# Kernel tuning notes

Hardware: AMD Instinct MI355X
Metric: run time of the kernel (lower is better)

The kernel has to match this reference:

```python
import jax, jax.numpy as jnp
import numpy as np

D_MODEL, D_K, D_V, H = 1024, 64, 64, 16
B, N = 4, 2048


def setup_inputs() -> dict:
    key = jax.random.key(0)
    ks = jax.random.split(key, 11)
    s = 0.02
    return {
        "Q": jax.random.normal(ks[0], (B, N, D_MODEL), jnp.float32),
        "K": jax.random.normal(ks[1], (B, N, D_MODEL), jnp.float32),
        "V": jax.random.normal(ks[2], (B, N, D_MODEL), jnp.float32),
        # stacked per-head projection weights: [h, d_model, d_k]
        "Wq": jax.random.normal(ks[3], (H, D_MODEL, D_K), jnp.float32) * s,
        "bq": jax.random.normal(ks[4], (H, D_K), jnp.float32) * s,
        "Wk": jax.random.normal(ks[5], (H, D_MODEL, D_K), jnp.float32) * s,
        "bk": jax.random.normal(ks[6], (H, D_K), jnp.float32) * s,
        "Wv": jax.random.normal(ks[7], (H, D_MODEL, D_V), jnp.float32) * s,
        "bv": jax.random.normal(ks[8], (H, D_V), jnp.float32) * s,
        "Wo": jax.random.normal(ks[9], (H * D_V, D_MODEL), jnp.float32) * s,
        "bo": jax.random.normal(ks[10], (D_MODEL,), jnp.float32) * s,
        "apply_mask": 1,
    }


def reference(Q, K, V, Wq, bq, Wk, bk, Wv, bv, Wo, bo, apply_mask):
    # fused per-head projections: [b, h, n, d_k]
    q = jnp.einsum("bnd,hdk->bhnk", Q, Wq) + bq[None, :, None, :]
    k = jnp.einsum("bnd,hdk->bhnk", K, Wk) + bk[None, :, None, :]
    v = jnp.einsum("bnd,hdv->bhnv", V, Wv) + bv[None, :, None, :]
    scores = jnp.einsum("bhnk,bhmk->bhnm", q, k) / jnp.sqrt(
        jnp.asarray(D_K, q.dtype)
    )
    if apply_mask:
        n = Q.shape[1]
        causal = jnp.tril(jnp.ones((n, n), dtype=bool))
        scores = jnp.where(causal[None, None], scores, -jnp.inf)
    weights = jax.nn.softmax(scores, axis=-1)
    out = jnp.einsum("bhnm,bhmv->bhnv", weights, v)
    # concat heads: [b, n, h*d_v]
    out = out.transpose(0, 2, 1, 3).reshape(Q.shape[0], Q.shape[1], H * D_V)
    return out @ Wo + bo
```

## Files before the change

### kernel.cpp

```cpp
#include <hip/hip_runtime.h>
#include <hip/hip_bf16.h>

#define H 16
#define DM 1024
#define DK 64
#define B_ 4
#define N_ 2048

typedef __attribute__((ext_vector_type(8))) short bf16x8;
typedef __attribute__((ext_vector_type(4))) short s16x4;
typedef __attribute__((ext_vector_type(2))) unsigned int u32x2;
typedef __attribute__((ext_vector_type(4))) float f32x4;

static __device__ __forceinline__ short f2bs(float x) {
    __hip_bfloat16 b = __float2bfloat16(x);
    return *reinterpret_cast<short*>(&b);
}

static __device__ __forceinline__ void async16(const void* g, void* l) {
    __builtin_amdgcn_global_load_lds(
        (const __attribute__((address_space(1))) void*)g,
        (__attribute__((address_space(3))) void*)l, 16, 0, 0);
}

static __device__ __forceinline__ unsigned packbf(float lo, float hi) {
    return __builtin_amdgcn_perm(__float_as_uint(hi), __float_as_uint(lo), 0x07060302u);
}

__global__ __launch_bounds__(256) void prep_kernel(
    const float* __restrict__ Q, const float* __restrict__ K, const float* __restrict__ V,
    const float* __restrict__ Wq, const float* __restrict__ Wk,
    const float* __restrict__ Wv, const float* __restrict__ Wo,
    short* __restrict__ Qb, short* __restrict__ Kb, short* __restrict__ Vb,
    short* __restrict__ wqT, short* __restrict__ wkT,
    short* __restrict__ wvT, short* __restrict__ woT)
{
    int y = blockIdx.y;
    if (y < 3) {
        const float* s = (y == 0) ? Q : (y == 1) ? K : V;
        short* d = (y == 0) ? Qb : (y == 1) ? Kb : Vb;
        size_t i = ((size_t)blockIdx.x * 256 + threadIdx.x) * 8;
        f32x4 a = *(const f32x4*)(s + i);
        f32x4 b = *(const f32x4*)(s + i + 4);
        bf16x8 p;
        #pragma unroll
        for (int j = 0; j < 4; ++j) { p[j] = f2bs(a[j]); p[4 + j] = f2bs(b[j]); }
        *(bf16x8*)(d + i) = p;
        return;
    }
    if (blockIdx.x >= 1024) return;
    __shared__ float tile[64][65];
    int z = blockIdx.x >> 8;
    int bx = blockIdx.x & 255;
    int t = threadIdx.x;
    int tj = t & 63, ti = t >> 6;

    if (z < 3) {
        const float* src = (z == 0) ? Wq : (z == 1) ? Wk : Wv;
        short* dst = (z == 0) ? wqT : (z == 1) ? wkT : wvT;
        int h = bx >> 4;
        int dmt = bx & 15;
        #pragma unroll
        for (int r = 0; r < 16; ++r) {
            int i = r * 4 + ti;
            tile[i][tj] = src[((size_t)h * 1024 + dmt * 64 + i) * 64 + tj];
        }
        __syncthreads();
        #pragma unroll
        for (int r = 0; r < 16; ++r) {
            int dk = r * 4 + ti;
            dst[((size_t)h * 64 + dk) * 1024 + dmt * 64 + tj] = f2bs(tile[tj][dk]);
        }
    } else {
        int kt = bx >> 4;
        int nt = bx & 15;
        #pragma unroll
        for (int r = 0; r < 16; ++r) {
            int i = r * 4 + ti;
            tile[i][tj] = Wo[((size_t)kt * 64 + i) * 1024 + nt * 64 + tj];
        }
        __syncthreads();
        #pragma unroll
        for (int r = 0; r < 16; ++r) {
            int jn = r * 4 + ti;
            woT[((size_t)nt * 64 + jn) * 1024 + kt * 64 + tj] = f2bs(tile[tj][jn]);
        }
    }
}

static __device__ __forceinline__ void gemm_mainloop(
    const short* __restrict__ A, const short* __restrict__ BT,
    int rowM0, int colN0, char* lds, f32x4 (&acc)[4][4])
{
    int tid = threadIdx.x;
    int lane = tid & 63, w = tid >> 6;
    int l16 = lane & 15, quad = lane >> 4;
    int wm = w >> 1, wn = w & 1;
    int xg = (quad ^ ((l16 >> 1) & 3)) << 4;

    int r0 = w * 32 + (lane >> 2);
    int gsl = ((lane & 3) ^ ((lane >> 3) & 3)) << 4;
    int dst0 = w * 2048 + lane * 16;
    const char* Ag0 = (const char*)A + (size_t)(rowM0 + r0) * 2048 + gsl;
    const char* Ag1 = Ag0 + 16 * 2048;
    const char* Bg0 = (const char*)BT + (size_t)(colN0 + r0) * 2048 + gsl;
    const char* Bg1 = Bg0 + 16 * 2048;

    #pragma unroll
    for (int t = 0; t < 2; ++t) {
        size_t kb = (size_t)t * 64;
        char* As = lds + t * 16384;
        char* Bs = As + 8192;
        async16(Ag0 + kb, As + dst0);
        async16(Ag1 + kb, As + dst0 + 1024);
        async16(Bg0 + kb, Bs + dst0);
        async16(Bg1 + kb, Bs + dst0 + 1024);
    }

    int c0 = 0;
    int cr = 32768;
    for (int it = 0; it < 32; ++it) {
        if (it < 31) asm volatile("s_waitcnt vmcnt(4)" ::: "memory");
        else         asm volatile("s_waitcnt vmcnt(0)" ::: "memory");
        __builtin_amdgcn_s_barrier();
        __builtin_amdgcn_sched_barrier(0);

        if (it + 2 < 32) {
            size_t kb = (size_t)(it + 2) * 64;
            char* Aw = lds + cr;
            char* Bw = Aw + 8192;
            async16(Ag0 + kb, Aw + dst0);
            async16(Ag1 + kb, Aw + dst0 + 1024);
            async16(Bg0 + kb, Bw + dst0);
            async16(Bg1 + kb, Bw + dst0 + 1024);
        }
        __builtin_amdgcn_sched_barrier(0);

        const char* As = lds + c0;
        const char* Bs = As + 8192;
        bf16x8 a[4], b[4];
        #pragma unroll
        for (int i = 0; i < 4; ++i)
            a[i] = *(const bf16x8*)(As + (wm * 64 + i * 16 + l16) * 64 + xg);
        #pragma unroll
        for (int j = 0; j < 4; ++j)
            b[j] = *(const bf16x8*)(Bs + (wn * 64 + j * 16 + l16) * 64 + xg);
        #pragma unroll
        for (int i = 0; i < 4; ++i)
            #pragma unroll
            for (int j = 0; j < 4; ++j)
                acc[i][j] = __builtin_amdgcn_mfma_f32_16x16x32_bf16(a[i], b[j], acc[i][j], 0, 0, 0);

        c0 += 16384; if (c0 == 49152) c0 = 0;
        cr += 16384; if (cr == 49152) cr = 0;
    }
}

__global__ __launch_bounds__(256) void proj_gemm(
    const short* __restrict__ Qb, const short* __restrict__ Kb, const short* __restrict__ Vb,
    const short* __restrict__ wqT, const short* __restrict__ wkT, const short* __restrict__ wvT,
    const float* __restrict__ bq, const float* __restrict__ bk, const float* __restrict__ bv,
    short* __restrict__ qbuf, short* __restrict__ kbuf, short* __restrict__ vTbuf)
{
    __shared__ char lds[49152];
    int which = blockIdx.z;
    const short* A  = (which == 0) ? Qb : (which == 1) ? Kb : Vb;
    const short* BT = (which == 0) ? wqT : (which == 1) ? wkT : wvT;
    const float* bias = (which == 0) ? bq : (which == 1) ? bk : bv;

    int rowM0 = blockIdx.x * 128;
    int colN0 = blockIdx.y * 128;

    f32x4 acc[4][4];
    #pragma unroll
    for (int i = 0; i < 4; ++i)
        #pragma unroll
        for (int j = 0; j < 4; ++j) acc[i][j] = (f32x4){0.f, 0.f, 0.f, 0.f};

    gemm_mainloop(A, BT, rowM0, colN0, lds, acc);

    int lane = threadIdx.x & 63, w = threadIdx.x >> 6;
    int l16 = lane & 15, quad = lane >> 4;
    int wm = w >> 1, wn = w & 1;

    if (which == 2) {
        #pragma unroll
        for (int j = 0; j < 4; ++j) {
            int col = colN0 + wn * 64 + j * 16 + l16;
            int hh = col >> 6, dv = col & 63;
            float bs = bias[col];
            #pragma unroll
            for (int i = 0; i < 4; ++i) {
                int rowb = rowM0 + wm * 64 + i * 16 + quad * 4;
                int bb = rowb >> 11, n0 = rowb & 2047;
                s16x4 pk;
                #pragma unroll
                for (int r2 = 0; r2 < 4; ++r2) pk[r2] = f2bs(acc[i][j][r2] + bs);
                *(s16x4*)(vTbuf + (((size_t)bb * H + hh) * DK + dv) * N_ + n0) = pk;
            }
        }
    } else {
        short* dst = (which == 0) ? qbuf : kbuf;
        float scl = (which == 0) ? 0.180336880f : 1.0f;
        #pragma unroll
        for (int j = 0; j < 4; ++j) {
            int col = colN0 + wn * 64 + j * 16 + l16;
            float bs = bias[col];
            #pragma unroll
            for (int i = 0; i < 4; ++i) {
                int rowb = rowM0 + wm * 64 + i * 16 + quad * 4;
                #pragma unroll
                for (int r2 = 0; r2 < 4; ++r2)
                    dst[(size_t)(rowb + r2) * 1024 + col] = f2bs((acc[i][j][r2] + bs) * scl);
            }
        }
    }
}

__global__ __launch_bounds__(256) void out_gemm(
    const short* __restrict__ obuf, const short* __restrict__ woT,
    const float* __restrict__ bo, float* __restrict__ out)
{
    __shared__ char lds[49152];
    int rowM0 = blockIdx.x * 128;
    int colN0 = blockIdx.y * 128;

    f32x4 acc[4][4];
    #pragma unroll
    for (int i = 0; i < 4; ++i)
        #pragma unroll
        for (int j = 0; j < 4; ++j) acc[i][j] = (f32x4){0.f, 0.f, 0.f, 0.f};

    gemm_mainloop(obuf, woT, rowM0, colN0, lds, acc);

    int lane = threadIdx.x & 63, w = threadIdx.x >> 6;
    int l16 = lane & 15, quad = lane >> 4;
    int wm = w >> 1, wn = w & 1;

    #pragma unroll
    for (int j = 0; j < 4; ++j) {
        int col = colN0 + wn * 64 + j * 16 + l16;
        float bs = bo[col];
        #pragma unroll
        for (int i = 0; i < 4; ++i) {
            int rowb = rowM0 + wm * 64 + i * 16 + quad * 4;
            #pragma unroll
            for (int r2 = 0; r2 < 4; ++r2)
                out[(size_t)(rowb + r2) * 1024 + col] = acc[i][j][r2] + bs;
        }
    }
}

__global__ __launch_bounds__(256) void flash_kernel(
    const short* __restrict__ qbuf, const short* __restrict__ kbuf, const short* __restrict__ vT,
    short* __restrict__ obuf, const int* __restrict__ amask)
{
    __shared__ short Ks[2][4096];
    __shared__ short Vs[2][4096];
    __shared__ char  plds[4][2048];

    int bid = blockIdx.x;
    int g = bid & 7, idx = bid >> 3;
    int bh = g * 8 + (idx >> 4);
    int xq = idx & 15;
    int b = bh >> 4, h = bh & 15;

    int tid = threadIdx.x;
    int lane = tid & 63, wave = tid >> 6;
    int l16 = lane & 15, quad = lane >> 4;
    int msk = amask[0];

    int i8 = lane >> 3, i7 = lane & 7;
    int sg = (i7 ^ i8) << 4;
    int pk0 = i8 * 4 + wave;
    int skey = wave * 16 + i8;
    int ldst = wave * 2048 + lane * 16;

    const char* kbase = (const char*)(kbuf + (size_t)b * 2048 * 1024 + h * 64);
    const char* vbase = (const char*)(vT + ((size_t)(b * 16 + h) * 64) * 2048);

    int m7 = l16 & 7;
    int g0 = (quad ^ m7) << 4;
    int g1 = ((4 | quad) ^ m7) << 4;

    char* pw = plds[wave];
    int prd0 = l16 * 128 + g0;
    int prd1 = l16 * 128 + g1;
    int pwa[4];
    #pragma unroll
    for (int r = 0; r < 4; ++r) {
        int row = quad * 4 + r;
        pwa[r] = row * 128 + (((l16 >> 1) ^ (row & 7)) << 4) + ((l16 & 1) << 3);
    }

    for (int pass = 0; pass < 2; ++pass) {
        int qt = pass ? (31 - xq) : xq;
        int qw = qt * 64 + wave * 16;
        int nkb = msk ? (qt + 1) : 32;

        const short* qp = qbuf + ((size_t)(b * 2048 + qw + l16)) * 1024 + h * 64;
        bf16x8 aq0 = *(const bf16x8*)(qp + quad * 8);
        bf16x8 aq1 = *(const bf16x8*)(qp + 32 + quad * 8);

        f32x4 o[4];
        float lsum[4];
        #pragma unroll
        for (int i = 0; i < 4; ++i) { o[i] = (f32x4){0.f, 0.f, 0.f, 0.f}; lsum[i] = 0.f; }

        async16(kbase + (size_t)pk0 * 2048 + sg, (char*)Ks[0] + ldst);
        async16(kbase + (size_t)(pk0 + 32) * 2048 + sg, (char*)Ks[0] + ldst + 1024);
        async16(vbase + (size_t)skey * 4096 + sg, (char*)Vs[0] + ldst);
        async16(vbase + (size_t)(skey + 8) * 4096 + sg, (char*)Vs[0] + ldst + 1024);

        for (int ib = 0; ib < nkb; ++ib) {
            __syncthreads();
            int cur = ib & 1;
            if (ib + 1 < nkb) {
                int nb = (ib + 1) & 1;
                size_t kb2 = (size_t)(ib + 1) * 64;
                async16(kbase + (kb2 + pk0) * 2048 + sg, (char*)Ks[nb] + ldst);
                async16(kbase + (kb2 + pk0 + 32) * 2048 + sg, (char*)Ks[nb] + ldst + 1024);
                async16(vbase + (size_t)skey * 4096 + kb2 * 2 + sg, (char*)Vs[nb] + ldst);
                async16(vbase + (size_t)(skey + 8) * 4096 + kb2 * 2 + sg, (char*)Vs[nb] + ldst + 1024);
            }
            int kb = ib * 64;

            f32x4 s[4];
            __builtin_amdgcn_s_setprio(1);
            #pragma unroll
            for (int nt = 0; nt < 4; ++nt) {
                const char* kr = (const char*)Ks[cur] + (nt * 16 + l16) * 128;
                bf16x8 b0 = *(const bf16x8*)(kr + g0);
                bf16x8 b1 = *(const bf16x8*)(kr + g1);
                f32x4 t = (f32x4){0.f, 0.f, 0.f, 0.f};
                t = __builtin_amdgcn_mfma_f32_16x16x32_bf16(aq0, b0, t, 0, 0, 0);
                t = __builtin_amdgcn_mfma_f32_16x16x32_bf16(aq1, b1, t, 0, 0, 0);
                s[nt] = t;
            }
            __builtin_amdgcn_s_setprio(0);

            if (msk && (kb + 63 > qw)) {
                #pragma unroll
                for (int r = 0; r < 4; ++r) {
                    int row = qw + quad * 4 + r;
                    #pragma unroll
                    for (int nt = 0; nt < 4; ++nt) {
                        int col = kb + l16 * 4 + nt;
                        if (col > row) s[nt][r] = -3e38f;
                    }
                }
            }

            __builtin_amdgcn_wave_barrier();
            #pragma unroll
            for (int r = 0; r < 4; ++r) {
                float p0 = __builtin_amdgcn_exp2f(s[0][r]);
                float p1 = __builtin_amdgcn_exp2f(s[1][r]);
                float p2 = __builtin_amdgcn_exp2f(s[2][r]);
                float p3 = __builtin_amdgcn_exp2f(s[3][r]);
                lsum[r] += (p0 + p1) + (p2 + p3);
                u32x2 pk;
                pk[0] = packbf(p0, p1);
                pk[1] = packbf(p2, p3);
                *(u32x2*)(pw + pwa[r]) = pk;
            }
            __builtin_amdgcn_wave_barrier();
            bf16x8 ap0 = *(const bf16x8*)(pw + prd0);
            bf16x8 ap1 = *(const bf16x8*)(pw + prd1);
            __builtin_amdgcn_wave_barrier();

            __builtin_amdgcn_s_setprio(1);
            #pragma unroll
            for (int vb = 0; vb < 4; ++vb) {
                const char* vr = (const char*)Vs[cur] + (vb * 16 + l16) * 128;
                bf16x8 v0 = *(const bf16x8*)(vr + g0);
                bf16x8 v1 = *(const bf16x8*)(vr + g1);
                o[vb] = __builtin_amdgcn_mfma_f32_16x16x32_bf16(ap0, v0, o[vb], 0, 0, 0);
                o[vb] = __builtin_amdgcn_mfma_f32_16x16x32_bf16(ap1, v1, o[vb], 0, 0, 0);
            }
            __builtin_amdgcn_s_setprio(0);
        }

        #pragma unroll
        for (int r = 0; r < 4; ++r) {
            float t = lsum[r];
            #pragma unroll
            for (int off = 1; off < 16; off <<= 1) t += __shfl_xor(t, off, 64);
            float inv = 1.0f / t;
            int row = qw + quad * 4 + r;
            #pragma unroll
            for (int vb = 0; vb < 4; ++vb)
                obuf[((size_t)(b * 2048 + row)) * 1024 + h * 64 + vb * 16 + l16] =
                    f2bs(o[vb][r] * inv);
        }
        __syncthreads();
    }
}

extern "C" void kernel_launch(void* const* d_in, const int* in_sizes, int n_in,
                              void* d_out, int out_size, void* d_ws, size_t ws_size,
                              hipStream_t stream)
{
    const float* Q  = (const float*)d_in[0];
    const float* K  = (const float*)d_in[1];
    const float* V  = (const float*)d_in[2];
    const float* Wq = (const float*)d_in[3];
    const float* bq = (const float*)d_in[4];
    const float* Wk = (const float*)d_in[5];
    const float* bk = (const float*)d_in[6];
    const float* Wv = (const float*)d_in[7];
    const float* bv = (const float*)d_in[8];
    const float* Wo = (const float*)d_in[9];
    const float* bo = (const float*)d_in[10];
    const int* amask = (const int*)d_in[11];
    float* out = (float*)d_out;

    char* ws = (char*)d_ws;
    const size_t SZ = (size_t)B_ * N_ * DM * sizeof(short);
    const size_t SZW = (size_t)H * DK * DM * sizeof(short);
    short* Qb    = (short*)ws; ws += SZ;
    short* Kb    = (short*)ws; ws += SZ;
    short* Vb    = (short*)ws; ws += SZ;
    short* qbuf  = (short*)ws; ws += SZ;
    short* kbuf  = (short*)ws; ws += SZ;
    short* vTbuf = (short*)ws; ws += SZ;
    short* wqT   = (short*)ws; ws += SZW;
    short* wkT   = (short*)ws; ws += SZW;
    short* wvT   = (short*)ws; ws += SZW;
    short* woT   = (short*)ws; ws += SZW;
    short* obuf  = Qb;

    prep_kernel<<<dim3(4096, 4), dim3(256), 0, stream>>>(Q, K, V, Wq, Wk, Wv, Wo,
                                                         Qb, Kb, Vb, wqT, wkT, wvT, woT);
    proj_gemm<<<dim3(64, 8, 3), dim3(256), 0, stream>>>(Qb, Kb, Vb, wqT, wkT, wvT,
                                                        bq, bk, bv, qbuf, kbuf, vTbuf);
    flash_kernel<<<dim3(1024), dim3(256), 0, stream>>>(qbuf, kbuf, vTbuf, obuf, amask);
    out_gemm<<<dim3(64, 8), dim3(256), 0, stream>>>(obuf, woT, bo, out);
}
```

Baseline: 314.6 us.

## Use 256x256 tiles with 512-thread blocks for projection GEMM

Replaces the 128x128, 256-thread projection GEMM with a 256x256 tile computed by 8 waves, each owning a 128x64 sub-tile with 8x4 MFMA accumulators. The triple-buffered LDS ring grows to 96 KB. This raises arithmetic intensity per loaded byte and halves global traffic per output. The cost is fewer blocks (384 instead of 1536) on a 256-CU device, more registers per thread, and lower occupancy.

After: 329.5 us. 4.7% more time.

```diff
diff --git a/kernel.cpp b/kernel.cpp
--- a/kernel.cpp
+++ b/kernel.cpp
@@ -84,6 +84,134 @@
         for (int r = 0; r < 16; ++r) {
             int jn = r * 4 + ti;
             woT[((size_t)nt * 64 + jn) * 1024 + kt * 64 + tj] = f2bs(tile[tj][jn]);
+        }
+    }
+}
+
+static __device__ __forceinline__ void gemm_mainloop256(
+    const short* __restrict__ A, const short* __restrict__ BT,
+    int rowM0, int colN0, char* lds, f32x4 (&acc)[8][4])
+{
+    int tid = threadIdx.x;
+    int lane = tid & 63, w = tid >> 6;
+    int l16 = lane & 15, quad = lane >> 4;
+    int wm = w >> 2, wn = w & 3;
+    int xg = (quad ^ ((l16 >> 1) & 3)) << 4;
+
+    int r0 = w * 32 + (lane >> 2);
+    int gsl = ((lane & 3) ^ ((lane >> 3) & 3)) << 4;
+    int dst0 = w * 2048 + lane * 16;
+    const char* Ag0 = (const char*)A + (size_t)(rowM0 + r0) * 2048 + gsl;
+    const char* Ag1 = Ag0 + 16 * 2048;
+    const char* Bg0 = (const char*)BT + (size_t)(colN0 + r0) * 2048 + gsl;
+    const char* Bg1 = Bg0 + 16 * 2048;
+
+    #pragma unroll
+    for (int t = 0; t < 2; ++t) {
+        size_t kb = (size_t)t * 64;
+        char* As = lds + t * 32768;
+        char* Bs = As + 16384;
+        async16(Ag0 + kb, As + dst0);
+        async16(Ag1 + kb, As + dst0 + 1024);
+        async16(Bg0 + kb, Bs + dst0);
+        async16(Bg1 + kb, Bs + dst0 + 1024);
+    }
+
+    int c0 = 0;
+    int cr = 65536;
+    for (int it = 0; it < 32; ++it) {
+        if (it < 31) asm volatile("s_waitcnt vmcnt(4)" ::: "memory");
+        else         asm volatile("s_waitcnt vmcnt(0)" ::: "memory");
+        __builtin_amdgcn_s_barrier();
+        __builtin_amdgcn_sched_barrier(0);
+
+        if (it + 2 < 32) {
+            size_t kb = (size_t)(it + 2) * 64;
+            char* Aw = lds + cr;
+            char* Bw = Aw + 16384;
+            async16(Ag0 + kb, Aw + dst0);
+            async16(Ag1 + kb, Aw + dst0 + 1024);
+            async16(Bg0 + kb, Bw + dst0);
+            async16(Bg1 + kb, Bw + dst0 + 1024);
+        }
+        __builtin_amdgcn_sched_barrier(0);
+
+        const char* As = lds + c0;
+        const char* Bs = As + 16384;
+        bf16x8 b[4];
+        #pragma unroll
+        for (int j = 0; j < 4; ++j)
+            b[j] = *(const bf16x8*)(Bs + (wn * 64 + j * 16 + l16) * 64 + xg);
+        #pragma unroll
+        for (int m = 0; m < 8; ++m) {
+            bf16x8 a = *(const bf16x8*)(As + (wm * 128 + m * 16 + l16) * 64 + xg);
+            #pragma unroll
+            for (int j = 0; j < 4; ++j)
+                acc[m][j] = __builtin_amdgcn_mfma_f32_16x16x32_bf16(a, b[j], acc[m][j], 0, 0, 0);
+        }
+
+        c0 += 32768; if (c0 == 98304) c0 = 0;
+        cr += 32768; if (cr == 98304) cr = 0;
+    }
+}
+
+__global__ __launch_bounds__(512) void proj_gemm(
+    const short* __restrict__ Qb, const short* __restrict__ Kb, const short* __restrict__ Vb,
+    const short* __restrict__ wqT, const short* __restrict__ wkT, const short* __restrict__ wvT,
+    const float* __restrict__ bq, const float* __restrict__ bk, const float* __restrict__ bv,
+    short* __restrict__ qbuf, short* __restrict__ kbuf, short* __restrict__ vTbuf)
+{
+    __shared__ char lds[98304];
+    int which = blockIdx.z;
+    const short* A  = (which == 0) ? Qb : (which == 1) ? Kb : Vb;
+    const short* BT = (which == 0) ? wqT : (which == 1) ? wkT : wvT;
+    const float* bias = (which == 0) ? bq : (which == 1) ? bk : bv;
+
+    int rowM0 = blockIdx.x * 256;
+    int colN0 = blockIdx.y * 256;
+
+    f32x4 acc[8][4];
+    #pragma unroll
+    for (int i = 0; i < 8; ++i)
+        #pragma unroll
+        for (int j = 0; j < 4; ++j) acc[i][j] = (f32x4){0.f, 0.f, 0.f, 0.f};
+
+    gemm_mainloop256(A, BT, rowM0, colN0, lds, acc);
+
+    int lane = threadIdx.x & 63, w = threadIdx.x >> 6;
+    int l16 = lane & 15, quad = lane >> 4;
+    int wm = w >> 2, wn = w & 3;
+
+    if (which == 2) {
+        #pragma unroll
+        for (int j = 0; j < 4; ++j) {
+            int col = colN0 + wn * 64 + j * 16 + l16;
+            int hh = col >> 6, dv = col & 63;
+            float bs = bias[col];
+            #pragma unroll
+            for (int m = 0; m < 8; ++m) {
+                int rowb = rowM0 + wm * 128 + m * 16 + quad * 4;
+                int bb = rowb >> 11, n0 = rowb & 2047;
+                s16x4 pk;
+                #pragma unroll
+                for (int r2 = 0; r2 < 4; ++r2) pk[r2] = f2bs(acc[m][j][r2] + bs);
+                *(s16x4*)(vTbuf + (((size_t)bb * H + hh) * DK + dv) * N_ + n0) = pk;
+            }
+        }
+    } else {
+        short* dst = (which == 0) ? qbuf : kbuf;
+        float scl = (which == 0) ? 0.180336880f : 1.0f;
+        #pragma unroll
+        for (int j = 0; j < 4; ++j) {
+            int col = colN0 + wn * 64 + j * 16 + l16;
+            float bs = bias[col];
+            #pragma unroll
+            for (int m = 0; m < 8; ++m) {
+                int rowb = rowM0 + wm * 128 + m * 16 + quad * 4;
+                #pragma unroll
+                for (int r2 = 0; r2 < 4; ++r2)
+                    dst[(size_t)(rowb + r2) * 1024 + col] = f2bs((acc[m][j][r2] + bs) * scl);
+            }
         }
     }
 }
@@ -153,67 +281,6 @@
 
         c0 += 16384; if (c0 == 49152) c0 = 0;
         cr += 16384; if (cr == 49152) cr = 0;
-    }
-}
-
-__global__ __launch_bounds__(256) void proj_gemm(
-    const short* __restrict__ Qb, const short* __restrict__ Kb, const short* __restrict__ Vb,
-    const short* __restrict__ wqT, const short* __restrict__ wkT, const short* __restrict__ wvT,
-    const float* __restrict__ bq, const float* __restrict__ bk, const float* __restrict__ bv,
-    short* __restrict__ qbuf, short* __restrict__ kbuf, short* __restrict__ vTbuf)
-{
-    __shared__ char lds[49152];
-    int which = blockIdx.z;
-    const short* A  = (which == 0) ? Qb : (which == 1) ? Kb : Vb;
-    const short* BT = (which == 0) ? wqT : (which == 1) ? wkT : wvT;
-    const float* bias = (which == 0) ? bq : (which == 1) ? bk : bv;
-
-    int rowM0 = blockIdx.x * 128;
-    int colN0 = blockIdx.y * 128;
-
-    f32x4 acc[4][4];
-    #pragma unroll
-    for (int i = 0; i < 4; ++i)
-        #pragma unroll
-        for (int j = 0; j < 4; ++j) acc[i][j] = (f32x4){0.f, 0.f, 0.f, 0.f};
-
-    gemm_mainloop(A, BT, rowM0, colN0, lds, acc);
-
-    int lane = threadIdx.x & 63, w = threadIdx.x >> 6;
-    int l16 = lane & 15, quad = lane >> 4;
-    int wm = w >> 1, wn = w & 1;
-
-    if (which == 2) {
-        #pragma unroll
-        for (int j = 0; j < 4; ++j) {
-            int col = colN0 + wn * 64 + j * 16 + l16;
-            int hh = col >> 6, dv = col & 63;
-            float bs = bias[col];
-            #pragma unroll
-            for (int i = 0; i < 4; ++i) {
-                int rowb = rowM0 + wm * 64 + i * 16 + quad * 4;
-                int bb = rowb >> 11, n0 = rowb & 2047;
-                s16x4 pk;
-                #pragma unroll
-                for (int r2 = 0; r2 < 4; ++r2) pk[r2] = f2bs(acc[i][j][r2] + bs);
-                *(s16x4*)(vTbuf + (((size_t)bb * H + hh) * DK + dv) * N_ + n0) = pk;
-            }
-        }
-    } else {
-        short* dst = (which == 0) ? qbuf : kbuf;
-        float scl = (which == 0) ? 0.180336880f : 1.0f;
-        #pragma unroll
-        for (int j = 0; j < 4; ++j) {
-            int col = colN0 + wn * 64 + j * 16 + l16;
-            float bs = bias[col];
-            #pragma unroll
-            for (int i = 0; i < 4; ++i) {
-                int rowb = rowM0 + wm * 64 + i * 16 + quad * 4;
-                #pragma unroll
-                for (int r2 = 0; r2 < 4; ++r2)
-                    dst[(size_t)(rowb + r2) * 1024 + col] = f2bs((acc[i][j][r2] + bs) * scl);
-            }
-        }
     }
 }
 
@@ -432,7 +499,7 @@
 
     prep_kernel<<<dim3(4096, 4), dim3(256), 0, stream>>>(Q, K, V, Wq, Wk, Wv, Wo,
                                                          Qb, Kb, Vb, wqT, wkT, wvT, woT);
-    proj_gemm<<<dim3(64, 8, 3), dim3(256), 0, stream>>>(Qb, Kb, Vb, wqT, wkT, wvT,
+    proj_gemm<<<dim3(32, 4, 3), dim3(512), 0, stream>>>(Qb, Kb, Vb, wqT, wkT, wvT,
                                                         bq, bk, bv, qbuf, kbuf, vTbuf);
     flash_kernel<<<dim3(1024), dim3(256), 0, stream>>>(qbuf, kbuf, vTbuf, obuf, amask);
     out_gemm<<<dim3(64, 8), dim3(256), 0, stream>>>(obuf, woT, bo, out);
```

## Rewrite projection GEMM with 256x256 tiles and phased double-buffered pipeline

Applied to the files above, without the earlier changes.

Replaces the 128x128, 256-thread projection GEMM with a 256x256, 512-thread kernel. It uses a double-buffered 128 KB LDS with K-steps of 128 and splits each step into four quadrant phases. Each phase issues async global-to-LDS loads for the next stage, then runs MFMAs at raised wave priority. The aim is more data reuse per LDS byte and better overlap of loads with compute. The trade-offs are fewer blocks (384 on the GPU, about 1.5 waves per CU) and heavy LDS use that allows only one block per CU.

Result: slower. 326.8 us (+3.9%).

```diff
diff --git a/kernel.cpp b/kernel.cpp
--- a/kernel.cpp
+++ b/kernel.cpp
@@ -84,6 +84,177 @@
         for (int r = 0; r < 16; ++r) {
             int jn = r * 4 + ti;
             woT[((size_t)nt * 64 + jn) * 1024 + kt * 64 + tj] = f2bs(tile[tj][jn]);
+        }
+    }
+}
+
+static __device__ __forceinline__ void gemm_8phase256(
+    const short* __restrict__ A, const short* __restrict__ BT,
+    int rowM0, int colN0, char* lds, f32x4 (&acc)[4][4][2])
+{
+    int tid = threadIdx.x;
+    int lane = tid & 63, w = tid >> 6;
+    int l16 = lane & 15, lq = lane >> 4;
+    int wm = w >> 2, wn = w & 3;
+    int xg = (lq ^ ((l16 >> 1) & 3)) << 4;
+
+    int sr = w * 16 + (lane >> 2);
+    int gsl = ((lane & 3) ^ ((lane >> 3) & 3)) << 4;
+    int sdst = w * 1024 + lane * 16;
+
+    const char* Asrc0 = (const char*)A  + (size_t)(rowM0 + sr) * 2048 + gsl;
+    const char* Asrc1 = Asrc0 + (size_t)128 * 2048;
+    const char* Bsrc0 = (const char*)BT + (size_t)(colN0 + sr) * 2048 + gsl;
+    const char* Bsrc1 = Bsrc0 + (size_t)128 * 2048;
+
+    async16(Asrc0,      lds + 0     + sdst);
+    async16(Asrc0 + 64, lds + 0     + sdst + 8192);
+    async16(Bsrc0,      lds + 32768 + sdst);
+    async16(Bsrc0 + 64, lds + 32768 + sdst + 8192);
+    async16(Bsrc1,      lds + 49152 + sdst);
+    async16(Bsrc1 + 64, lds + 49152 + sdst + 8192);
+    async16(Asrc1,      lds + 16384 + sdst);
+    async16(Asrc1 + 64, lds + 16384 + sdst + 8192);
+    asm volatile("s_waitcnt vmcnt(4)" ::: "memory");
+    __builtin_amdgcn_s_barrier();
+    __builtin_amdgcn_sched_barrier(0);
+
+    for (int t = 0; t < 16; ++t) {
+        const char* Ab = lds + (t & 1) * 65536;
+        const char* Bb = Ab + 32768;
+        char* Sb = lds + ((t + 1) & 1) * 65536;
+        int kn = (t + 1) * 128;
+        bool st = (t + 1) < 16;
+
+        #pragma unroll
+        for (int q = 0; q < 4; ++q) {
+            int mq = q >> 1, nq = q & 1;
+
+            bf16x8 af[4][2], bfv[2][2];
+            #pragma unroll
+            for (int m2 = 0; m2 < 4; ++m2) {
+                int r = wm * 64 + m2 * 16 + l16;
+                #pragma unroll
+                for (int j = 0; j < 2; ++j)
+                    af[m2][j] = *(const bf16x8*)(Ab + mq * 16384 + j * 8192 + r * 64 + xg);
+            }
+            #pragma unroll
+            for (int n2 = 0; n2 < 2; ++n2) {
+                int c = wn * 32 + n2 * 16 + l16;
+                #pragma unroll
+                for (int j = 0; j < 2; ++j)
+                    bfv[n2][j] = *(const bf16x8*)(Bb + nq * 16384 + j * 8192 + c * 64 + xg);
+            }
+
+            if (st) {
+                if (q == 0) {
+                    async16(Asrc0 + kn,      Sb + 0     + sdst);
+                    async16(Asrc0 + kn + 64, Sb + 0     + sdst + 8192);
+                } else if (q == 1) {
+                    async16(Bsrc0 + kn,      Sb + 32768 + sdst);
+                    async16(Bsrc0 + kn + 64, Sb + 32768 + sdst + 8192);
+                } else if (q == 2) {
+                    async16(Bsrc1 + kn,      Sb + 49152 + sdst);
+                    async16(Bsrc1 + kn + 64, Sb + 49152 + sdst + 8192);
+                } else {
+                    async16(Asrc1 + kn,      Sb + 16384 + sdst);
+                    async16(Asrc1 + kn + 64, Sb + 16384 + sdst + 8192);
+                }
+            }
+
+            if (st) {
+                if (q != 2) asm volatile("s_waitcnt vmcnt(4)" ::: "memory");
+            } else {
+                if (q == 0)      asm volatile("s_waitcnt vmcnt(2)" ::: "memory");
+                else if (q == 1) asm volatile("s_waitcnt vmcnt(0)" ::: "memory");
+            }
+            __builtin_amdgcn_s_barrier();
+            __builtin_amdgcn_sched_barrier(0);
+
+            __builtin_amdgcn_s_setprio(1);
+            #pragma unroll
+            for (int m2 = 0; m2 < 4; ++m2)
+                #pragma unroll
+                for (int n2 = 0; n2 < 2; ++n2)
+                    #pragma unroll
+                    for (int j = 0; j < 2; ++j)
+                        acc[q][m2][n2] = __builtin_amdgcn_mfma_f32_16x16x32_bf16(
+                            af[m2][j], bfv[n2][j], acc[q][m2][n2], 0, 0, 0);
+            __builtin_amdgcn_s_setprio(0);
+            __builtin_amdgcn_sched_barrier(0);
+            __builtin_amdgcn_s_barrier();
+            __builtin_amdgcn_sched_barrier(0);
+        }
+    }
+}
+
+__global__ __launch_bounds__(512, 2) void proj_gemm(
+    const short* __restrict__ Qb, const short* __restrict__ Kb, const short* __restrict__ Vb,
+    const short* __restrict__ wqT, const short* __restrict__ wkT, const short* __restrict__ wvT,
+    const float* __restrict__ bq, const float* __restrict__ bk, const float* __restrict__ bv,
+    short* __restrict__ qbuf, short* __restrict__ kbuf, short* __restrict__ vTbuf)
+{
+    __shared__ char lds[131072];
+    int which = blockIdx.z;
+    const short* A  = (which == 0) ? Qb : (which == 1) ? Kb : Vb;
+    const short* BT = (which == 0) ? wqT : (which == 1) ? wkT : wvT;
+    const float* bias = (which == 0) ? bq : (which == 1) ? bk : bv;
+
+    int rowM0 = blockIdx.x * 256;
+    int colN0 = blockIdx.y * 256;
+
+    f32x4 acc[4][4][2];
+    #pragma unroll
+    for (int a = 0; a < 4; ++a)
+        #pragma unroll
+        for (int b = 0; b < 4; ++b)
+            #pragma unroll
+            for (int c = 0; c < 2; ++c) acc[a][b][c] = (f32x4){0.f, 0.f, 0.f, 0.f};
+
+    gemm_8phase256(A, BT, rowM0, colN0, lds, acc);
+
+    int lane = threadIdx.x & 63, w = threadIdx.x >> 6;
+    int l16 = lane & 15, lq = lane >> 4;
+    int wm = w >> 2, wn = w & 3;
+
+    if (which == 2) {
+        #pragma unroll
+        for (int qd = 0; qd < 4; ++qd) {
+            int mq = qd >> 1, nq = qd & 1;
+            #pragma unroll
+            for (int n2 = 0; n2 < 2; ++n2) {
+                int col = colN0 + nq * 128 + wn * 32 + n2 * 16 + l16;
+                int hh = col >> 6, dv = col & 63;
+                float bs = bias[col];
+                #pragma unroll
+                for (int m2 = 0; m2 < 4; ++m2) {
+                    int rowb = rowM0 + mq * 128 + wm * 64 + m2 * 16 + lq * 4;
+                    int bb = rowb >> 11, n0 = rowb & 2047;
+                    s16x4 pk;
+                    #pragma unroll
+                    for (int r2 = 0; r2 < 4; ++r2) pk[r2] = f2bs(acc[qd][m2][n2][r2] + bs);
+                    *(s16x4*)(vTbuf + (((size_t)bb * H + hh) * DK + dv) * N_ + n0) = pk;
+                }
+            }
+        }
+    } else {
+        short* dst = (which == 0) ? qbuf : kbuf;
+        float scl = (which == 0) ? 0.180336880f : 1.0f;
+        #pragma unroll
+        for (int qd = 0; qd < 4; ++qd) {
+            int mq = qd >> 1, nq = qd & 1;
+            #pragma unroll
+            for (int n2 = 0; n2 < 2; ++n2) {
+                int col = colN0 + nq * 128 + wn * 32 + n2 * 16 + l16;
+                float bs = bias[col];
+                #pragma unroll
+                for (int m2 = 0; m2 < 4; ++m2) {
+                    int rowb = rowM0 + mq * 128 + wm * 64 + m2 * 16 + lq * 4;
+                    #pragma unroll
+                    for (int r2 = 0; r2 < 4; ++r2)
+                        dst[(size_t)(rowb + r2) * 1024 + col] = f2bs((acc[qd][m2][n2][r2] + bs) * scl);
+                }
+            }
         }
     }
 }
@@ -153,67 +324,6 @@
 
         c0 += 16384; if (c0 == 49152) c0 = 0;
         cr += 16384; if (cr == 49152) cr = 0;
-    }
-}
-
-__global__ __launch_bounds__(256) void proj_gemm(
-    const short* __restrict__ Qb, const short* __restrict__ Kb, const short* __restrict__ Vb,
-    const short* __restrict__ wqT, const short* __restrict__ wkT, const short* __restrict__ wvT,
-    const float* __restrict__ bq, const float* __restrict__ bk, const float* __restrict__ bv,
-    short* __restrict__ qbuf, short* __restrict__ kbuf, short* __restrict__ vTbuf)
-{
-    __shared__ char lds[49152];
-    int which = blockIdx.z;
-    const short* A  = (which == 0) ? Qb : (which == 1) ? Kb : Vb;
-    const short* BT = (which == 0) ? wqT : (which == 1) ? wkT : wvT;
-    const float* bias = (which == 0) ? bq : (which == 1) ? bk : bv;
-
-    int rowM0 = blockIdx.x * 128;
-    int colN0 = blockIdx.y * 128;
-
-    f32x4 acc[4][4];
-    #pragma unroll
-    for (int i = 0; i < 4; ++i)
-        #pragma unroll
-        for (int j = 0; j < 4; ++j) acc[i][j] = (f32x4){0.f, 0.f, 0.f, 0.f};
-
-    gemm_mainloop(A, BT, rowM0, colN0, lds, acc);
-
-    int lane = threadIdx.x & 63, w = threadIdx.x >> 6;
-    int l16 = lane & 15, quad = lane >> 4;
-    int wm = w >> 1, wn = w & 1;
-
-    if (which == 2) {
-        #pragma unroll
-        for (int j = 0; j < 4; ++j) {
-            int col = colN0 + wn * 64 + j * 16 + l16;
-            int hh = col >> 6, dv = col & 63;
-            float bs = bias[col];
-            #pragma unroll
-            for (int i = 0; i < 4; ++i) {
-                int rowb = rowM0 + wm * 64 + i * 16 + quad * 4;
-                int bb = rowb >> 11, n0 = rowb & 2047;
-                s16x4 pk;
-                #pragma unroll
-                for (int r2 = 0; r2 < 4; ++r2) pk[r2] = f2bs(acc[i][j][r2] + bs);
-                *(s16x4*)(vTbuf + (((size_t)bb * H + hh) * DK + dv) * N_ + n0) = pk;
-            }
-        }
-    } else {
-        short* dst = (which == 0) ? qbuf : kbuf;
-        float scl = (which == 0) ? 0.180336880f : 1.0f;
-        #pragma unroll
-        for (int j = 0; j < 4; ++j) {
-            int col = colN0 + wn * 64 + j * 16 + l16;
-            float bs = bias[col];
-            #pragma unroll
-            for (int i = 0; i < 4; ++i) {
-                int rowb = rowM0 + wm * 64 + i * 16 + quad * 4;
-                #pragma unroll
-                for (int r2 = 0; r2 < 4; ++r2)
-                    dst[(size_t)(rowb + r2) * 1024 + col] = f2bs((acc[i][j][r2] + bs) * scl);
-            }
-        }
     }
 }
 
@@ -432,7 +542,7 @@
 
     prep_kernel<<<dim3(4096, 4), dim3(256), 0, stream>>>(Q, K, V, Wq, Wk, Wv, Wo,
                                                          Qb, Kb, Vb, wqT, wkT, wvT, woT);
-    proj_gemm<<<dim3(64, 8, 3), dim3(256), 0, stream>>>(Qb, Kb, Vb, wqT, wkT, wvT,
+    proj_gemm<<<dim3(32, 4, 3), dim3(512), 0, stream>>>(Qb, Kb, Vb, wqT, wkT, wvT,
                                                         bq, bk, bv, qbuf, kbuf, vTbuf);
     flash_kernel<<<dim3(1024), dim3(256), 0, stream>>>(qbuf, kbuf, vTbuf, obuf, amask);
     out_gemm<<<dim3(64, 8), dim3(256), 0, stream>>>(obuf, woT, bo, out);
```
